# Kernel tuning notes

Hardware: AMD Instinct MI355X
Metric: run time of the kernel (lower is better)

The kernel has to match this reference:

```python
import jax, jax.numpy as jnp
import numpy as np

BLOCKSIZE = 4096
OUT_FEATURES = 16384
IN_FEATURES = 4096
BATCH, SEQ = 4, 2048


def setup_inputs() -> dict:
    key = jax.random.key(0)
    k_x, k_w, k_a, k_b = jax.random.split(key, 4)
    x = jax.random.normal(k_x, (BATCH, SEQ, IN_FEATURES), dtype=jnp.float32)
    # quantized int8 weight stored as indices into the 256-entry codebook
    weight_q = jax.random.randint(k_w, (OUT_FEATURES, IN_FEATURES), 0, 256, dtype=jnp.int32)
    n_blocks = (OUT_FEATURES * IN_FEATURES) // BLOCKSIZE  # 16384
    absmax = jax.random.uniform(k_a, (n_blocks,), dtype=jnp.float32) + 0.5
    # bitsandbytes dynamic-map code: a sorted table of values in [-1, 1]
    code = jnp.linspace(-1.0, 1.0, 256, dtype=jnp.float32)
    bias = jax.random.normal(k_b, (OUT_FEATURES,), dtype=jnp.float32) * 0.02
    return {"x": x, "weight_q": weight_q, "absmax": absmax, "code": code, "bias": bias}


def dequantize_blockwise(weight_q, absmax, code):
    # codebook lookup then per-block absmax scaling
    flat = code[weight_q.reshape(-1)]                      # [out*in]
    flat = flat.reshape(-1, BLOCKSIZE) * absmax[:, None]   # [n_blocks, blocksize]
    return flat.reshape(weight_q.shape)                    # [out, in]


def reference(x, weight_q, absmax, code, bias):
    w = dequantize_blockwise(weight_q, absmax, code)       # [out, in] fp32
    # F.linear(x, w, bias) = x @ w.T + bias
    return jnp.einsum("bsi,oi->bso", x, w) + bias
```

## Files before the change

### kernel.cpp

```cpp
#include <hip/hip_runtime.h>
#include <hip/hip_bf16.h>
#include <stdint.h>

#define M_TOTAL 8192
#define N_TOTAL 16384
#define K_TOTAL 4096

#define BM 256
#define BN 256
#define BK 64
#define NKT (K_TOTAL / BK)

using f32x4  = __attribute__((ext_vector_type(4))) float;
using bf16x8 = __attribute__((ext_vector_type(8))) short;

#define UNROLL _Pragma("unroll")

__device__ __forceinline__ unsigned short f2bf(float f) {
    union { float f; unsigned u; } v; v.f = f;
    unsigned r = v.u + 0x7fffu + ((v.u >> 16) & 1u);
    return (unsigned short)(r >> 16);
}

__device__ __forceinline__ void gload_lds16(const void* g, void* l) {
    __builtin_amdgcn_global_load_lds(
        (const __attribute__((address_space(1))) unsigned int*)g,
        (__attribute__((address_space(3))) unsigned int*)l,
        16, 0, 0);
}

__global__ void dequant_w_kernel(const int* __restrict__ q,
                                 const float* __restrict__ am,
                                 const float* __restrict__ code,
                                 unsigned short* __restrict__ wb) {
    __shared__ float lc[256];
    if (threadIdx.x < 256) lc[threadIdx.x] = code[threadIdx.x];
    __syncthreads();
    const int total = (N_TOTAL / 4) * K_TOTAL;
    const int stride = gridDim.x * blockDim.x;
    for (int i = blockIdx.x * blockDim.x + threadIdx.x; i < total; i += stride) {
        int4 v = reinterpret_cast<const int4*>(q)[i];
        float a = am[i >> 10];
        ushort4 o;
        o.x = f2bf(lc[v.x & 255] * a);
        o.y = f2bf(lc[v.y & 255] * a);
        o.z = f2bf(lc[v.z & 255] * a);
        o.w = f2bf(lc[v.w & 255] * a);
        reinterpret_cast<ushort4*>(wb)[i] = o;
    }
}

__global__ void cvt_x_kernel(const float* __restrict__ x,
                             unsigned short* __restrict__ xb) {
    const int total = (M_TOTAL * K_TOTAL) / 4;
    const int stride = gridDim.x * blockDim.x;
    for (int i = blockIdx.x * blockDim.x + threadIdx.x; i < total; i += stride) {
        float4 v = reinterpret_cast<const float4*>(x)[i];
        ushort4 o;
        o.x = f2bf(v.x); o.y = f2bf(v.y); o.z = f2bf(v.z); o.w = f2bf(v.w);
        reinterpret_cast<ushort4*>(xb)[i] = o;
    }
}

#define LOAD_A(BUFI, MH)                                                          \
    UNROLL for (int mf = 0; mf < 4; ++mf)                                         \
        UNROLL for (int ks = 0; ks < 2; ++ks)                                     \
            a_r[mf][ks] = *reinterpret_cast<const bf16x8*>(                       \
                &sA[BUFI][((MH)*128 + arow_base + mf*16)*BK +                     \
                          (((ks*4 + rslot_hi) ^ rslot_xor)*8)]);

#define LOAD_B(BUFI, NH)                                                          \
    UNROLL for (int nf = 0; nf < 2; ++nf)                                         \
        UNROLL for (int ks = 0; ks < 2; ++ks)                                     \
            b_r[nf][ks] = *reinterpret_cast<const bf16x8*>(                       \
                &sB[BUFI][((NH)*128 + brow_base + nf*16)*BK +                     \
                          (((ks*4 + rslot_hi) ^ rslot_xor)*8)]);

#define DO_MFMA(MH, NH)                                                           \
    UNROLL for (int mf = 0; mf < 4; ++mf)                                         \
        UNROLL for (int nf = 0; nf < 2; ++nf) {                                   \
            acc[MH][mf][NH][nf] = __builtin_amdgcn_mfma_f32_16x16x32_bf16(        \
                a_r[mf][0], b_r[nf][0], acc[MH][mf][NH][nf], 0, 0, 0);            \
            acc[MH][mf][NH][nf] = __builtin_amdgcn_mfma_f32_16x16x32_bf16(        \
                a_r[mf][1], b_r[nf][1], acc[MH][mf][NH][nf], 0, 0, 0);            \
        }

#define PHASE_MID()                                                               \
    __builtin_amdgcn_s_barrier();                                                 \
    asm volatile("s_waitcnt lgkmcnt(0)" ::: "memory");                            \
    __builtin_amdgcn_s_setprio(1);

#define PHASE_END()                                                               \
    __builtin_amdgcn_s_setprio(0);                                                \
    __builtin_amdgcn_s_barrier();

__global__ __launch_bounds__(512, 2) void gemm8_kernel(
        const unsigned short* __restrict__ A,
        const unsigned short* __restrict__ B,
        const float* __restrict__ bias,
        float* __restrict__ C) {
    __shared__ __align__(16) unsigned short sA[2][BM * BK];
    __shared__ __align__(16) unsigned short sB[2][BN * BK];

    const int nwg = gridDim.x;
    const int bid = blockIdx.x;
    const int wg  = (bid & 7) * (nwg >> 3) + (bid >> 3);
    const int nbn = N_TOTAL / BN;
    const int brow = (wg / nbn) * BM;
    const int bcol = (wg % nbn) * BN;

    const int tid  = threadIdx.x;
    const int wid  = tid >> 6;
    const int lane = tid & 63;
    const int wm   = wid >> 2;
    const int wn   = wid & 3;

    const int srow = wid * 8 + (lane >> 3);
    const int scol = ((lane & 7) ^ (lane >> 3)) * 8;
    const unsigned short* Asrc = A + (long long)(brow + srow) * K_TOTAL + scol;
    const unsigned short* Bsrc = B + (long long)(bcol + srow) * K_TOTAL + scol;

    auto stA = [&](int h, int j, int kt, int b) {
        gload_lds16(Asrc + (long long)(h*128 + j*64) * K_TOTAL + kt*BK,
                    &sA[b][(h*128 + j*64)*BK + wid*512]);
    };
    auto stB = [&](int h, int j, int kt, int b) {
        gload_lds16(Bsrc + (long long)(h*128 + j*64) * K_TOTAL + kt*BK,
                    &sB[b][(h*128 + j*64)*BK + wid*512]);
    };

    const int arow_base = wm * 64 + (lane & 15);
    const int brow_base = wn * 32 + (lane & 15);
    const int rslot_hi  = lane >> 4;
    const int rslot_xor = lane & 7;

    f32x4 acc[2][4][2][2];
    UNROLL for (int mh = 0; mh < 2; ++mh)
        UNROLL for (int mf = 0; mf < 4; ++mf)
            UNROLL for (int nh = 0; nh < 2; ++nh)
                UNROLL for (int nf = 0; nf < 2; ++nf)
                    acc[mh][mf][nh][nf] = (f32x4){0.f, 0.f, 0.f, 0.f};

    bf16x8 a_r[4][2];
    bf16x8 b_r[2][2];

    stA(0,0,0,0); stA(0,1,0,0); stA(1,0,0,0); stA(1,1,0,0);
    stB(0,0,0,0); stB(0,1,0,0); stB(1,0,0,0); stB(1,1,0,0);
    stA(0,0,1,1); stA(0,1,1,1);
    stB(1,0,1,1); stB(1,1,1,1);
    asm volatile("s_waitcnt vmcnt(4)" ::: "memory");
    __builtin_amdgcn_s_barrier();

    for (int it = 0; it < NKT/2; ++it) {
        const int t   = 2*it;
        const int tp1 = t + 1;
        const int p2  = (t+2 < NKT) ? t+2 : NKT-1;
        const int p3  = (t+3 < NKT) ? t+3 : NKT-1;

        LOAD_A(0, 0); LOAD_B(0, 0);
        stA(1,0,tp1,1); stA(1,1,tp1,1);
        PHASE_MID(); DO_MFMA(0, 0); PHASE_END();

        LOAD_B(0, 1);
        stB(0,0,tp1,1); stB(0,1,tp1,1);
        PHASE_MID(); DO_MFMA(0, 1); PHASE_END();

        LOAD_A(0, 1);
        stA(0,0,p2,0); stA(0,1,p2,0);
        PHASE_MID(); DO_MFMA(1, 1); PHASE_END();

        LOAD_B(0, 0);
        stB(1,0,p2,0); stB(1,1,p2,0);
        PHASE_MID(); DO_MFMA(1, 0);
        __builtin_amdgcn_s_setprio(0);
        asm volatile("s_waitcnt vmcnt(4)" ::: "memory");
        __builtin_amdgcn_s_barrier();

        LOAD_A(1, 0); LOAD_B(1, 0);
        stA(1,0,p2,0); stA(1,1,p2,0);
        PHASE_MID(); DO_MFMA(0, 0); PHASE_END();

        LOAD_B(1, 1);
        stB(0,0,p2,0); stB(0,1,p2,0);
        PHASE_MID(); DO_MFMA(0, 1); PHASE_END();

        LOAD_A(1, 1);
        stA(0,0,p3,1); stA(0,1,p3,1);
        PHASE_MID(); DO_MFMA(1, 1); PHASE_END();

        LOAD_B(1, 0);
        stB(1,0,p3,1); stB(1,1,p3,1);
        PHASE_MID(); DO_MFMA(1, 0);
        __builtin_amdgcn_s_setprio(0);
        asm volatile("s_waitcnt vmcnt(4)" ::: "memory");
        __builtin_amdgcn_s_barrier();
    }

    const int crow0 = (lane >> 4) * 4;
    const int ccol  = lane & 15;
    UNROLL for (int mh = 0; mh < 2; ++mh)
        UNROLL for (int mf = 0; mf < 4; ++mf) {
            const long long row0 = (long long)brow + mh*128 + wm*64 + mf*16 + crow0;
            UNROLL for (int nh = 0; nh < 2; ++nh)
                UNROLL for (int nf = 0; nf < 2; ++nf) {
                    const int col = bcol + nh*128 + wn*32 + nf*16 + ccol;
                    const float bv = bias[col];
                    UNROLL for (int r = 0; r < 4; ++r)
                        C[(row0 + r) * N_TOTAL + col] = acc[mh][mf][nh][nf][r] + bv;
                }
        }
}

extern "C" void kernel_launch(void* const* d_in, const int* in_sizes, int n_in,
                              void* d_out, int out_size, void* d_ws, size_t ws_size,
                              hipStream_t stream) {
    const float* x      = (const float*)d_in[0];
    const int*   wq     = (const int*)  d_in[1];
    const float* absmax = (const float*)d_in[2];
    const float* code   = (const float*)d_in[3];
    const float* bias   = (const float*)d_in[4];
    float* out = (float*)d_out;

    unsigned short* wb = (unsigned short*)d_ws;
    unsigned short* xb = wb + (size_t)N_TOTAL * K_TOTAL;

    dequant_w_kernel<<<2048, 256, 0, stream>>>(wq, absmax, code, wb);
    cvt_x_kernel   <<<2048, 256, 0, stream>>>(x, xb);

    dim3 grid((M_TOTAL / BM) * (N_TOTAL / BN));
    gemm8_kernel<<<grid, 512, 0, stream>>>(xb, wb, bias, out);
}
```

Baseline: 1.228 ms.

## Restructure GEMM main loop with register double-buffered fragments and one barrier per tile

```diff
diff --git a/kernel.cpp b/kernel.cpp
--- a/kernel.cpp
+++ b/kernel.cpp
@@ -62,39 +62,30 @@
     }
 }
 
-#define LOAD_A(BUFI, MH)                                                          \
+#define LOAD_AH(DST, BUFI, MH)                                                    \
     UNROLL for (int mf = 0; mf < 4; ++mf)                                         \
         UNROLL for (int ks = 0; ks < 2; ++ks)                                     \
-            a_r[mf][ks] = *reinterpret_cast<const bf16x8*>(                       \
+            DST[mf][ks] = *reinterpret_cast<const bf16x8*>(                       \
                 &sA[BUFI][((MH)*128 + arow_base + mf*16)*BK +                     \
                           (((ks*4 + rslot_hi) ^ rslot_xor)*8)]);
 
-#define LOAD_B(BUFI, NH)                                                          \
+#define LOAD_BH(DST, BUFI, NH)                                                    \
     UNROLL for (int nf = 0; nf < 2; ++nf)                                         \
         UNROLL for (int ks = 0; ks < 2; ++ks)                                     \
-            b_r[nf][ks] = *reinterpret_cast<const bf16x8*>(                       \
+            DST[nf][ks] = *reinterpret_cast<const bf16x8*>(                       \
                 &sB[BUFI][((NH)*128 + brow_base + nf*16)*BK +                     \
                           (((ks*4 + rslot_hi) ^ rslot_xor)*8)]);
 
-#define DO_MFMA(MH, NH)                                                           \
+#define MFMA_Q(MH, NH, AR, BR)                                                    \
     UNROLL for (int mf = 0; mf < 4; ++mf)                                         \
         UNROLL for (int nf = 0; nf < 2; ++nf) {                                   \
             acc[MH][mf][NH][nf] = __builtin_amdgcn_mfma_f32_16x16x32_bf16(        \
-                a_r[mf][0], b_r[nf][0], acc[MH][mf][NH][nf], 0, 0, 0);            \
+                AR[mf][0], BR[nf][0], acc[MH][mf][NH][nf], 0, 0, 0);              \
             acc[MH][mf][NH][nf] = __builtin_amdgcn_mfma_f32_16x16x32_bf16(        \
-                a_r[mf][1], b_r[nf][1], acc[MH][mf][NH][nf], 0, 0, 0);            \
+                AR[mf][1], BR[nf][1], acc[MH][mf][NH][nf], 0, 0, 0);              \
         }
 
-#define PHASE_MID()                                                               \
-    __builtin_amdgcn_s_barrier();                                                 \
-    asm volatile("s_waitcnt lgkmcnt(0)" ::: "memory");                            \
-    __builtin_amdgcn_s_setprio(1);
-
-#define PHASE_END()                                                               \
-    __builtin_amdgcn_s_setprio(0);                                                \
-    __builtin_amdgcn_s_barrier();
-
-__global__ __launch_bounds__(512, 2) void gemm8_kernel(
+__global__ __launch_bounds__(512, 2) void gemm_rp_kernel(
         const unsigned short* __restrict__ A,
         const unsigned short* __restrict__ B,
         const float* __restrict__ bias,
@@ -128,6 +119,10 @@
         gload_lds16(Bsrc + (long long)(h*128 + j*64) * K_TOTAL + kt*BK,
                     &sB[b][(h*128 + j*64)*BK + wid*512]);
     };
+    auto stage_tile = [&](int kt, int b) {
+        stA(0,0,kt,b); stA(0,1,kt,b); stA(1,0,kt,b); stA(1,1,kt,b);
+        stB(0,0,kt,b); stB(0,1,kt,b); stB(1,0,kt,b); stB(1,1,kt,b);
+    };
 
     const int arow_base = wm * 64 + (lane & 15);
     const int brow_base = wn * 32 + (lane & 15);
@@ -141,59 +136,40 @@
                 UNROLL for (int nf = 0; nf < 2; ++nf)
                     acc[mh][mf][nh][nf] = (f32x4){0.f, 0.f, 0.f, 0.f};
 
-    bf16x8 a_r[4][2];
-    bf16x8 b_r[2][2];
-
-    stA(0,0,0,0); stA(0,1,0,0); stA(1,0,0,0); stA(1,1,0,0);
-    stB(0,0,0,0); stB(0,1,0,0); stB(1,0,0,0); stB(1,1,0,0);
-    stA(0,0,1,1); stA(0,1,1,1);
-    stB(1,0,1,1); stB(1,1,1,1);
-    asm volatile("s_waitcnt vmcnt(4)" ::: "memory");
+    bf16x8 a0_r[4][2], a1_r[4][2];
+    bf16x8 b0_r[2][2], b1_r[2][2];
+
+    stage_tile(0, 0);
+    stage_tile(1, 1);
+    asm volatile("s_waitcnt vmcnt(8)" ::: "memory");
     __builtin_amdgcn_s_barrier();
-
-    for (int it = 0; it < NKT/2; ++it) {
-        const int t   = 2*it;
-        const int tp1 = t + 1;
-        const int p2  = (t+2 < NKT) ? t+2 : NKT-1;
-        const int p3  = (t+3 < NKT) ? t+3 : NKT-1;
-
-        LOAD_A(0, 0); LOAD_B(0, 0);
-        stA(1,0,tp1,1); stA(1,1,tp1,1);
-        PHASE_MID(); DO_MFMA(0, 0); PHASE_END();
-
-        LOAD_B(0, 1);
-        stB(0,0,tp1,1); stB(0,1,tp1,1);
-        PHASE_MID(); DO_MFMA(0, 1); PHASE_END();
-
-        LOAD_A(0, 1);
-        stA(0,0,p2,0); stA(0,1,p2,0);
-        PHASE_MID(); DO_MFMA(1, 1); PHASE_END();
-
-        LOAD_B(0, 0);
-        stB(1,0,p2,0); stB(1,1,p2,0);
-        PHASE_MID(); DO_MFMA(1, 0);
+    LOAD_AH(a0_r, 0, 0);
+    LOAD_BH(b0_r, 0, 0);
+
+    for (int t = 0; t < NKT; ++t) {
+        const int b = t & 1;
+
+        LOAD_BH(b1_r, b, 1);
+        LOAD_AH(a1_r, b, 1);
+
+        __builtin_amdgcn_s_setprio(1);
+        MFMA_Q(0, 0, a0_r, b0_r);
+        MFMA_Q(0, 1, a0_r, b1_r);
+        MFMA_Q(1, 1, a1_r, b1_r);
         __builtin_amdgcn_s_setprio(0);
-        asm volatile("s_waitcnt vmcnt(4)" ::: "memory");
+
+        asm volatile("s_waitcnt lgkmcnt(0) vmcnt(0)" ::: "memory");
         __builtin_amdgcn_s_barrier();
 
-        LOAD_A(1, 0); LOAD_B(1, 0);
-        stA(1,0,p2,0); stA(1,1,p2,0);
-        PHASE_MID(); DO_MFMA(0, 0); PHASE_END();
-
-        LOAD_B(1, 1);
-        stB(0,0,p2,0); stB(0,1,p2,0);
-        PHASE_MID(); DO_MFMA(0, 1); PHASE_END();
-
-        LOAD_A(1, 1);
-        stA(0,0,p3,1); stA(0,1,p3,1);
-        PHASE_MID(); DO_MFMA(1, 1); PHASE_END();
-
-        LOAD_B(1, 0);
-        stB(1,0,p3,1); stB(1,1,p3,1);
-        PHASE_MID(); DO_MFMA(1, 0);
+        if (t + 2 < NKT) stage_tile(t + 2, b);
+
+        LOAD_AH(a0_r, b ^ 1, 0);
+
+        __builtin_amdgcn_s_setprio(1);
+        MFMA_Q(1, 0, a1_r, b0_r);
         __builtin_amdgcn_s_setprio(0);
-        asm volatile("s_waitcnt vmcnt(4)" ::: "memory");
-        __builtin_amdgcn_s_barrier();
+
+        LOAD_BH(b0_r, b ^ 1, 0);
     }
 
     const int crow0 = (lane >> 4) * 4;
@@ -228,5 +204,5 @@
     cvt_x_kernel   <<<2048, 256, 0, stream>>>(x, xb);
 
     dim3 grid((M_TOTAL / BM) * (N_TOTAL / BN));
-    gemm8_kernel<<<grid, 512, 0, stream>>>(xb, wb, bias, out);
-}
+    gemm_rp_kernel<<<grid, 512, 0, stream>>>(xb, wb, bias, out);
+}
```

Measured after the change: 1.278 ms. +4.1%, slower.
